# Kernel tuning notes

Measured on AMD Instinct MI355X. Metric: run time of the kernel, lower is better.

## Reference

```python
import jax, jax.numpy as jnp
import numpy as np

N, E = 20000, 320000
IN, HID, OUT, H = 128, 32, 1, 4
EPS = 1e-16  # PyG softmax epsilon


def _p(key, shape, scale=0.05):
    return jax.random.normal(key, shape, dtype=jnp.float32) * scale


def setup_inputs() -> dict:
    key = jax.random.key(0)
    ks = jax.random.split(key, 20)
    d = {
        "x": jax.random.normal(ks[0], (N, IN), dtype=jnp.float32),
        "edge_src": jax.random.randint(ks[1], (E,), 0, N, dtype=jnp.int32),
        "edge_dst": jax.random.randint(ks[2], (E,), 0, N, dtype=jnp.int32),
        # layer 1: TransformerConv(IN, HID, H)  ->  [N, H*HID]
        "W1q": _p(ks[3], (IN, H * HID)), "b1q": jnp.zeros((H * HID,), jnp.float32),
        "W1k": _p(ks[4], (IN, H * HID)), "b1k": jnp.zeros((H * HID,), jnp.float32),
        "W1v": _p(ks[5], (IN, H * HID)), "b1v": jnp.zeros((H * HID,), jnp.float32),
        "W1s": _p(ks[6], (IN, H * HID)), "b1s": jnp.zeros((H * HID,), jnp.float32),
        # layer 2: TransformerConv(H*HID, OUT, H) -> [N, H*OUT]
        "W2q": _p(ks[7], (H * HID, H * OUT)), "b2q": jnp.zeros((H * OUT,), jnp.float32),
        "W2k": _p(ks[8], (H * HID, H * OUT)), "b2k": jnp.zeros((H * OUT,), jnp.float32),
        "W2v": _p(ks[9], (H * HID, H * OUT)), "b2v": jnp.zeros((H * OUT,), jnp.float32),
        "W2s": _p(ks[10], (H * HID, H * OUT)), "b2s": jnp.zeros((H * OUT,), jnp.float32),
        # final nn.Linear(heads, 1)
        "Wl": _p(ks[11], (H, 1)), "bl": jnp.zeros((1,), jnp.float32),
    }
    return d


def transformer_conv(x, src, dst, Wq, bq, Wk, bk, Wv, bv, Ws, bs, heads, ch):
    n = x.shape[0]
    q = (x @ Wq + bq).reshape(n, heads, ch)
    k = (x @ Wk + bk).reshape(n, heads, ch)
    v = (x @ Wv + bv).reshape(n, heads, ch)
    qi, kj, vj = q[dst], k[src], v[src]            # [E,H,C] gathers
    score = (qi * kj).sum(-1) / jnp.sqrt(jnp.float32(ch))  # [E,H]
    m = jax.ops.segment_max(score, dst, num_segments=n)    # segment softmax by target
    e = jnp.exp(score - m[dst])
    s = jax.ops.segment_sum(e, dst, num_segments=n)
    alpha = e / (s[dst] + EPS)                              # [E,H]
    agg = jax.ops.segment_sum(alpha[:, :, None] * vj, dst, num_segments=n)  # [N,H,C]
    return agg.reshape(n, heads * ch) + x @ Ws + bs          # concat + root skip


def reference(x, edge_src, edge_dst,
              W1q, b1q, W1k, b1k, W1v, b1v, W1s, b1s,
              W2q, b2q, W2k, b2k, W2v, b2v, W2s, b2s,
              Wl, bl):
    h = transformer_conv(x, edge_src, edge_dst, W1q, b1q, W1k, b1k, W1v, b1v, W1s, b1s, H, HID)
    h = jax.nn.relu(h)  # dropout is identity in eval
    h = transformer_conv(h, edge_src, edge_dst, W2q, b2q, W2k, b2k, W2v, b2v, W2s, b2s, H, OUT)
    y = h @ Wl + bl                      # [N,1]
    return y.mean(axis=0, keepdims=True)  # [1,1]
```

## Files before the change

### kernel.cpp

```cpp
#include <hip/hip_runtime.h>
#include <math.h>

static constexpr float EPS_PYG = 1e-16f;
static constexpr float INV_SQRT32 = 0.17677669529663687f;

typedef short bf16x8 __attribute__((ext_vector_type(8)));
typedef float f32x4 __attribute__((ext_vector_type(4)));

__device__ inline unsigned short f2bf(float f) {
    union { float f; unsigned u; } x; x.f = f;
    unsigned r = x.u + 0x7FFFu + ((x.u >> 16) & 1u);
    return (unsigned short)(r >> 16);
}
__device__ inline float bf_hi(unsigned u) {
    union { unsigned u; float f; } x; x.u = u & 0xFFFF0000u; return x.f;
}
__device__ inline float bf_lo(unsigned u) {
    union { unsigned u; float f; } x; x.u = u << 16; return x.f;
}

__global__ void deg_slot_kernel(const int* __restrict__ dst, int* __restrict__ deg,
                                int* __restrict__ slot, int E) {
    int e = blockIdx.x * blockDim.x + threadIdx.x;
    if (e < E) slot[e] = atomicAdd(&deg[dst[e]], 1);
}

__global__ __launch_bounds__(1024) void scan_kernel(const int* __restrict__ deg,
                                                    int* __restrict__ row_off, int n,
                                                    float* __restrict__ out,
                                                    const float* __restrict__ bl) {
    const int t = threadIdx.x;
    const int CH = (n + 1023) >> 10;
    const int base = t * CH;
    int vals[32];
    int sum = 0;
#pragma unroll 4
    for (int i = 0; i < CH; ++i) {
        int idx = base + i;
        int v = (idx < n) ? deg[idx] : 0;
        sum += v;
        vals[i] = sum;
    }
    const int lane = t & 63;
    const int wid = t >> 6;
    int wsum = sum;
#pragma unroll
    for (int off = 1; off < 64; off <<= 1) {
        int o = __shfl_up(wsum, off, 64);
        if (lane >= off) wsum += o;
    }
    __shared__ int wtot[16];
    if (lane == 63) wtot[wid] = wsum;
    __syncthreads();
    if (t < 64) {
        int v = (t < 16) ? wtot[t] : 0;
        int inc = v;
#pragma unroll
        for (int off = 1; off < 16; off <<= 1) {
            int o = __shfl_up(inc, off, 64);
            if (t >= off) inc += o;
        }
        if (t < 16) wtot[t] = inc - v;
    }
    __syncthreads();
    const int toff = wtot[wid] + (wsum - sum);
    if (t == 0) { row_off[0] = 0; out[0] = bl[0]; }
#pragma unroll 4
    for (int i = 0; i < CH; ++i) {
        int idx = base + i;
        if (idx < n) row_off[idx + 1] = toff + vals[i];
    }
}

__global__ void scatter_kernel(const int* __restrict__ src, const int* __restrict__ dst,
                               const int* __restrict__ row_off, const int* __restrict__ slot,
                               int* __restrict__ csr_src, int E) {
    int e = blockIdx.x * blockDim.x + threadIdx.x;
    if (e < E) csr_src[row_off[dst[e]] + slot[e]] = src[e];
}

__global__ __launch_bounds__(256) void prep_kernel(
    const float4* __restrict__ X, ushort4* __restrict__ Xb, int total4,
    const float* __restrict__ Wq, const float* __restrict__ Wk,
    const float* __restrict__ Wv, const float* __restrict__ Wsk,
    unsigned short* __restrict__ Wbt)
{
    const int b = blockIdx.x;
    if (b < 4) {
        const float* W = (b == 0) ? Wq : (b == 1) ? Wk : (b == 2) ? Wv : Wsk;
        for (int i = threadIdx.x; i < 16384; i += 256) {
            int k = i >> 7, nn = i & 127;
            Wbt[b * 16384 + nn * 128 + k] = f2bf(W[i]);
        }
    } else {
        int i = (b - 4) * 256 + threadIdx.x;
        if (i < total4) {
            float4 v = X[i];
            ushort4 o;
            o.x = f2bf(v.x); o.y = f2bf(v.y); o.z = f2bf(v.z); o.w = f2bf(v.w);
            Xb[i] = o;
        }
    }
}

__global__ __launch_bounds__(256) void gemm1_mfma(
    const unsigned short* __restrict__ Xb, const unsigned short* __restrict__ Wbt,
    const float* __restrict__ bq, const float* __restrict__ bk,
    const float* __restrict__ bv, const float* __restrict__ bsk,
    float* __restrict__ Q, unsigned int* __restrict__ KV,
    float* __restrict__ S, int n)
{
    const int mode = blockIdx.y;

    const int tid  = threadIdx.x;
    const int wave = tid >> 6;
    const int lane = tid & 63;
    const int m    = lane & 15;
    const int quad = lane >> 4;
    const int r0   = blockIdx.x * 64 + wave * 16;

    int arow = r0 + m;
    if (arow >= n) arow = n - 1;

    if (mode == 1) {
        const unsigned short* WK = Wbt + 16384;
        const unsigned short* WV = Wbt + 2 * 16384;
        f32x4 accK[8] = {};
        f32x4 accV[8] = {};
#pragma unroll
        for (int kc = 0; kc < 128; kc += 32) {
            bf16x8 a = *(const bf16x8*)(Xb + (size_t)arow * 128 + kc + quad * 8);
#pragma unroll
            for (int ct = 0; ct < 8; ++ct) {
                bf16x8 bk8 = *(const bf16x8*)(WK + (ct * 16 + m) * 128 + kc + quad * 8);
                accK[ct] = __builtin_amdgcn_mfma_f32_16x16x32_bf16(a, bk8, accK[ct], 0, 0, 0);
                bf16x8 bv8 = *(const bf16x8*)(WV + (ct * 16 + m) * 128 + kc + quad * 8);
                accV[ct] = __builtin_amdgcn_mfma_f32_16x16x32_bf16(a, bv8, accV[ct], 0, 0, 0);
            }
        }
#pragma unroll
        for (int ct = 0; ct < 8; ++ct) {
            const int col = ct * 16 + m;
            const float bbk = bk[col], bbv = bv[col];
#pragma unroll
            for (int r = 0; r < 4; ++r) {
                const int row = r0 + quad * 4 + r;
                if (row < n) {
                    unsigned kb = f2bf(accK[ct][r] + bbk);
                    unsigned vb = f2bf(accV[ct][r] + bbv);
                    KV[(size_t)row * 128 + col] = (kb << 16) | vb;
                }
            }
        }
    } else {
        const int mat = (mode == 0) ? 0 : 3;
        const unsigned short* W = Wbt + (size_t)mat * 16384;
        const float* bias = (mode == 0) ? bq : bsk;
        float* C = (mode == 0) ? Q : S;
        f32x4 acc[8] = {};
#pragma unroll
        for (int kc = 0; kc < 128; kc += 32) {
            bf16x8 a = *(const bf16x8*)(Xb + (size_t)arow * 128 + kc + quad * 8);
#pragma unroll
            for (int ct = 0; ct < 8; ++ct) {
                bf16x8 bfr = *(const bf16x8*)(W + (ct * 16 + m) * 128 + kc + quad * 8);
                acc[ct] = __builtin_amdgcn_mfma_f32_16x16x32_bf16(a, bfr, acc[ct], 0, 0, 0);
            }
        }
#pragma unroll
        for (int ct = 0; ct < 8; ++ct) {
            const int col = ct * 16 + m;
            const float bb = bias[col];
#pragma unroll
            for (int r = 0; r < 4; ++r) {
                const int row = r0 + quad * 4 + r;
                if (row < n) C[(size_t)row * 128 + col] = acc[ct][r] + bb;
            }
        }
    }
}

__global__ __launch_bounds__(128) void l1_agg_kernel(
    const float* __restrict__ Q, const unsigned int* __restrict__ KV,
    const float* __restrict__ S,
    const int* __restrict__ row_off, const int* __restrict__ csr_src,
    float* __restrict__ H1, int n)
{
    const int node = blockIdx.x;
    const int t = threadIdx.x;
    const float q = Q[(size_t)node * 128 + t];
    const int beg = row_off[node], end = row_off[node + 1];

    float l = 0.f, acc = 0.f;
    int pos = beg;
    for (; pos + 4 <= end; pos += 4) {
        int s0 = csr_src[pos];
        int s1 = csr_src[pos + 1];
        int s2 = csr_src[pos + 2];
        int s3 = csr_src[pos + 3];
        unsigned u0 = KV[(size_t)s0 * 128 + t];
        unsigned u1 = KV[(size_t)s1 * 128 + t];
        unsigned u2 = KV[(size_t)s2 * 128 + t];
        unsigned u3 = KV[(size_t)s3 * 128 + t];
        float p0 = q * bf_hi(u0), p1 = q * bf_hi(u1);
        float p2 = q * bf_hi(u2), p3 = q * bf_hi(u3);
        p0 += __shfl_xor(p0, 16, 32); p1 += __shfl_xor(p1, 16, 32);
        p2 += __shfl_xor(p2, 16, 32); p3 += __shfl_xor(p3, 16, 32);
        p0 += __shfl_xor(p0, 8, 32);  p1 += __shfl_xor(p1, 8, 32);
        p2 += __shfl_xor(p2, 8, 32);  p3 += __shfl_xor(p3, 8, 32);
        p0 += __shfl_xor(p0, 4, 32);  p1 += __shfl_xor(p1, 4, 32);
        p2 += __shfl_xor(p2, 4, 32);  p3 += __shfl_xor(p3, 4, 32);
        p0 += __shfl_xor(p0, 2, 32);  p1 += __shfl_xor(p1, 2, 32);
        p2 += __shfl_xor(p2, 2, 32);  p3 += __shfl_xor(p3, 2, 32);
        p0 += __shfl_xor(p0, 1, 32);  p1 += __shfl_xor(p1, 1, 32);
        p2 += __shfl_xor(p2, 1, 32);  p3 += __shfl_xor(p3, 1, 32);
        float e0 = __expf(p0 * INV_SQRT32);
        float e1 = __expf(p1 * INV_SQRT32);
        float e2 = __expf(p2 * INV_SQRT32);
        float e3 = __expf(p3 * INV_SQRT32);
        l   += (e0 + e1) + (e2 + e3);
        acc += (e0 * bf_lo(u0) + e1 * bf_lo(u1)) + (e2 * bf_lo(u2) + e3 * bf_lo(u3));
    }
    for (; pos < end; ++pos) {
        int s0 = csr_src[pos];
        unsigned u0 = KV[(size_t)s0 * 128 + t];
        float p0 = q * bf_hi(u0);
        p0 += __shfl_xor(p0, 16, 32);
        p0 += __shfl_xor(p0, 8, 32);
        p0 += __shfl_xor(p0, 4, 32);
        p0 += __shfl_xor(p0, 2, 32);
        p0 += __shfl_xor(p0, 1, 32);
        float e0 = __expf(p0 * INV_SQRT32);
        l += e0;
        acc += e0 * bf_lo(u0);
    }
    float out = acc / (l + EPS_PYG) + S[(size_t)node * 128 + t];
    H1[(size_t)node * 128 + t] = fmaxf(out, 0.f);
}

__global__ __launch_bounds__(256) void gemm2_kernel(
    const float* __restrict__ H1,
    const float* __restrict__ Wq, const float* __restrict__ Wk,
    const float* __restrict__ Wv, const float* __restrict__ Wsk,
    const float* __restrict__ bq, const float* __restrict__ bk,
    const float* __restrict__ bv, const float* __restrict__ bsk,
    float4* __restrict__ Q2, float4* __restrict__ KV2, float4* __restrict__ S2, int n)
{
    __shared__ float Hs[64][129];
    __shared__ float Wt[128][16];
    __shared__ float bt[16];

    const int tid = threadIdx.x;
    const int r0 = blockIdx.x * 64;

    for (int i = tid; i < 2048; i += 256) {
        int row = i >> 4, col = i & 15;
        int mt = col >> 2, c = col & 3;
        const float* Wm = (mt == 0) ? Wq : (mt == 1) ? Wk : (mt == 2) ? Wv : Wsk;
        Wt[row][col] = Wm[row * 4 + c];
    }
    if (tid < 16) {
        int mt = tid >> 2;
        const float* bm = (mt == 0) ? bq : (mt == 1) ? bk : (mt == 2) ? bv : bsk;
        bt[tid] = bm[tid & 3];
    }
    for (int f = tid; f < 2048; f += 256) {
        int row = f >> 5, c4 = f & 31;
        float4 val = make_float4(0.f, 0.f, 0.f, 0.f);
        if (r0 + row < n) val = ((const float4*)H1)[(size_t)(r0 + row) * 32 + c4];
        Hs[row][c4 * 4 + 0] = val.x;
        Hs[row][c4 * 4 + 1] = val.y;
        Hs[row][c4 * 4 + 2] = val.z;
        Hs[row][c4 * 4 + 3] = val.w;
    }
    __syncthreads();

    const int nl = tid & 63;
    const int jg = tid >> 6;
    float a0 = 0.f, a1 = 0.f, a2 = 0.f, a3 = 0.f;
#pragma unroll 4
    for (int k = 0; k < 128; ++k) {
        float h = Hs[nl][k];
        a0 += h * Wt[k][jg * 4 + 0];
        a1 += h * Wt[k][jg * 4 + 1];
        a2 += h * Wt[k][jg * 4 + 2];
        a3 += h * Wt[k][jg * 4 + 3];
    }
    int node = r0 + nl;
    if (node < n) {
        float4 o = make_float4(a0 + bt[jg * 4 + 0], a1 + bt[jg * 4 + 1],
                               a2 + bt[jg * 4 + 2], a3 + bt[jg * 4 + 3]);
        if (jg == 0)      Q2[node] = o;
        else if (jg == 1) KV2[(size_t)node * 2 + 0] = o;
        else if (jg == 2) KV2[(size_t)node * 2 + 1] = o;
        else              S2[node] = o;
    }
}

__global__ __launch_bounds__(256) void l2_agg_kernel(
    const float4* __restrict__ Q2, const float4* __restrict__ KV2,
    const float4* __restrict__ S2,
    const int* __restrict__ row_off, const int* __restrict__ csr_src,
    const float* __restrict__ Wl, float* __restrict__ out, int n, float invn)
{
    const int t  = threadIdx.x;
    const int g  = t >> 4;
    const int gl = t & 15;
    const int nd = blockIdx.x * 16 + g;
    float y = 0.f;
    if (nd < n) {
        const int beg = row_off[nd], end = row_off[nd + 1];
        float4 q = Q2[nd];
        float l0 = 0.f, l1 = 0.f, l2 = 0.f, l3 = 0.f;
        float a0 = 0.f, a1 = 0.f, a2 = 0.f, a3 = 0.f;
        for (int pos = beg + gl; pos < end; pos += 16) {
            int src = csr_src[pos];
            float4 k = KV2[(size_t)src * 2 + 0];
            float4 v = KV2[(size_t)src * 2 + 1];
            float e0 = __expf(q.x * k.x);
            float e1 = __expf(q.y * k.y);
            float e2 = __expf(q.z * k.z);
            float e3 = __expf(q.w * k.w);
            l0 += e0; a0 += e0 * v.x;
            l1 += e1; a1 += e1 * v.y;
            l2 += e2; a2 += e2 * v.z;
            l3 += e3; a3 += e3 * v.w;
        }
#pragma unroll
        for (int mk = 8; mk >= 1; mk >>= 1) {
            l0 += __shfl_xor(l0, mk, 16); l1 += __shfl_xor(l1, mk, 16);
            l2 += __shfl_xor(l2, mk, 16); l3 += __shfl_xor(l3, mk, 16);
            a0 += __shfl_xor(a0, mk, 16); a1 += __shfl_xor(a1, mk, 16);
            a2 += __shfl_xor(a2, mk, 16); a3 += __shfl_xor(a3, mk, 16);
        }
        if (gl == 0) {
            float4 sk = S2[nd];
            float h0 = a0 / (l0 + EPS_PYG) + sk.x;
            float h1 = a1 / (l1 + EPS_PYG) + sk.y;
            float h2 = a2 / (l2 + EPS_PYG) + sk.z;
            float h3 = a3 / (l3 + EPS_PYG) + sk.w;
            y = (h0 * Wl[0] + h1 * Wl[1] + h2 * Wl[2] + h3 * Wl[3]) * invn;
        }
    }
    __shared__ float red[256];
    red[t] = y;
    __syncthreads();
    for (int off = 128; off > 0; off >>= 1) {
        if (t < (unsigned)off) red[t] += red[t + off];
        __syncthreads();
    }
    if (t == 0) atomicAdd(out, red[0]);
}

extern "C" void kernel_launch(void* const* d_in, const int* in_sizes, int n_in,
                              void* d_out, int out_size, void* d_ws, size_t ws_size,
                              hipStream_t stream) {
    const float* x        = (const float*)d_in[0];
    const int*   edge_src = (const int*)d_in[1];
    const int*   edge_dst = (const int*)d_in[2];
    const float* W1q = (const float*)d_in[3];  const float* b1q = (const float*)d_in[4];
    const float* W1k = (const float*)d_in[5];  const float* b1k = (const float*)d_in[6];
    const float* W1v = (const float*)d_in[7];  const float* b1v = (const float*)d_in[8];
    const float* W1s = (const float*)d_in[9];  const float* b1s = (const float*)d_in[10];
    const float* W2q = (const float*)d_in[11]; const float* b2q = (const float*)d_in[12];
    const float* W2k = (const float*)d_in[13]; const float* b2k = (const float*)d_in[14];
    const float* W2v = (const float*)d_in[15]; const float* b2v = (const float*)d_in[16];
    const float* W2s = (const float*)d_in[17]; const float* b2s = (const float*)d_in[18];
    const float* Wl  = (const float*)d_in[19]; const float* bl  = (const float*)d_in[20];

    const int N = in_sizes[0] / 128;
    const int E = in_sizes[1];
    float* out = (float*)d_out;

    float* ws  = (float*)d_ws;
    size_t off = 0;
    float*        Q1  = ws + off; off += (size_t)N * 128;
    unsigned int* KV  = (unsigned int*)(ws + off); off += (size_t)N * 128;
    float*        S1  = ws + off; off += (size_t)N * 128;
    float*        H1  = ws + off; off += (size_t)N * 128;
    float*        q2  = ws + off; off += (size_t)N * 4;
    float*        kv2 = ws + off; off += (size_t)N * 8;
    float*        s2  = ws + off; off += (size_t)N * 4;
    unsigned short* Xb  = (unsigned short*)(ws + off); off += (size_t)N * 64;
    unsigned short* Wbt = (unsigned short*)(ws + off); off += 4 * 16384 / 2;
    int* ibase   = (int*)(ws + off);
    int* deg     = ibase;
    int* row_off = ibase + N;
    int* slot    = ibase + 2 * N + 4;
    int* csr_src = slot + E;

    hipMemsetAsync(deg, 0, (size_t)N * sizeof(int), stream);
    deg_slot_kernel<<<(E + 255) / 256, 256, 0, stream>>>(edge_dst, deg, slot, E);
    scan_kernel<<<1, 1024, 0, stream>>>(deg, row_off, N, out, bl);
    scatter_kernel<<<(E + 255) / 256, 256, 0, stream>>>(edge_src, edge_dst, row_off,
                                                        slot, csr_src, E);

    const int total4 = N * 32;
    prep_kernel<<<4 + (total4 + 255) / 256, 256, 0, stream>>>(
        (const float4*)x, (ushort4*)Xb, total4, W1q, W1k, W1v, W1s, Wbt);

    {
        dim3 grid((N + 63) / 64, 3);
        gemm1_mfma<<<grid, 256, 0, stream>>>(Xb, Wbt, b1q, b1k, b1v, b1s,
                                             Q1, KV, S1, N);
    }
    l1_agg_kernel<<<N, 128, 0, stream>>>(Q1, KV, S1, row_off, csr_src, H1, N);

    gemm2_kernel<<<(N + 63) / 64, 256, 0, stream>>>(H1, W2q, W2k, W2v, W2s,
                                                    b2q, b2k, b2v, b2s,
                                                    (float4*)q2, (float4*)kv2,
                                                    (float4*)s2, N);
    l2_agg_kernel<<<(N + 15) / 16, 256, 0, stream>>>((const float4*)q2,
                                                     (const float4*)kv2,
                                                     (const float4*)s2,
                                                     row_off, csr_src, Wl, out, N,
                                                     1.0f / (float)N);
}
```

Baseline: 253.8 us.

## Merge graph-build and prep launches, vectorize layer-1 aggregation to 32 lanes per node

The degree/slot atomics are merged with the bf16 conversion of X and the weights into one launch. The CSR scatter is merged with the layer-1 MFMA GEMM into another, with the GEMM grid flattened onto blockIdx.x. This cuts four launches down to two and lets independent work overlap. The layer-1 aggregation now gives each node a 32-lane group, so 8 nodes share a block, and each lane loads 4 channels with uint4/float4 accesses. That shortens each per-edge dot-product reduction to 3 shuffles, at the cost of a smaller unroll and more registers per lane.

```diff
diff --git a/kernel.cpp b/kernel.cpp
--- a/kernel.cpp
+++ b/kernel.cpp
@@ -19,10 +19,35 @@
     union { unsigned u; float f; } x; x.u = u << 16; return x.f;
 }
 
-__global__ void deg_slot_kernel(const int* __restrict__ dst, int* __restrict__ deg,
-                                int* __restrict__ slot, int E) {
-    int e = blockIdx.x * blockDim.x + threadIdx.x;
-    if (e < E) slot[e] = atomicAdd(&deg[dst[e]], 1);
+__global__ __launch_bounds__(256) void build_prep_kernel(
+    const int* __restrict__ dst, int* __restrict__ deg, int* __restrict__ slot,
+    int E, int nblk_deg,
+    const float4* __restrict__ X, ushort4* __restrict__ Xb, int total4,
+    const float* __restrict__ Wq, const float* __restrict__ Wk,
+    const float* __restrict__ Wv, const float* __restrict__ Wsk,
+    unsigned short* __restrict__ Wbt)
+{
+    const int b = blockIdx.x;
+    const int t = threadIdx.x;
+    if (b < nblk_deg) {
+        int e = b * 256 + t;
+        if (e < E) slot[e] = atomicAdd(&deg[dst[e]], 1);
+    } else if (b < nblk_deg + 4) {
+        int m = b - nblk_deg;
+        const float* W = (m == 0) ? Wq : (m == 1) ? Wk : (m == 2) ? Wv : Wsk;
+        for (int i = t; i < 16384; i += 256) {
+            int k = i >> 7, nn = i & 127;
+            Wbt[m * 16384 + nn * 128 + k] = f2bf(W[i]);
+        }
+    } else {
+        int i = (b - nblk_deg - 4) * 256 + t;
+        if (i < total4) {
+            float4 v = X[i];
+            ushort4 o;
+            o.x = f2bf(v.x); o.y = f2bf(v.y); o.z = f2bf(v.z); o.w = f2bf(v.w);
+            Xb[i] = o;
+        }
+    }
 }
 
 __global__ __launch_bounds__(1024) void scan_kernel(const int* __restrict__ deg,
@@ -72,52 +97,32 @@
     }
 }
 
-__global__ void scatter_kernel(const int* __restrict__ src, const int* __restrict__ dst,
-                               const int* __restrict__ row_off, const int* __restrict__ slot,
-                               int* __restrict__ csr_src, int E) {
-    int e = blockIdx.x * blockDim.x + threadIdx.x;
-    if (e < E) csr_src[row_off[dst[e]] + slot[e]] = src[e];
-}
-
-__global__ __launch_bounds__(256) void prep_kernel(
-    const float4* __restrict__ X, ushort4* __restrict__ Xb, int total4,
-    const float* __restrict__ Wq, const float* __restrict__ Wk,
-    const float* __restrict__ Wv, const float* __restrict__ Wsk,
-    unsigned short* __restrict__ Wbt)
-{
-    const int b = blockIdx.x;
-    if (b < 4) {
-        const float* W = (b == 0) ? Wq : (b == 1) ? Wk : (b == 2) ? Wv : Wsk;
-        for (int i = threadIdx.x; i < 16384; i += 256) {
-            int k = i >> 7, nn = i & 127;
-            Wbt[b * 16384 + nn * 128 + k] = f2bf(W[i]);
-        }
-    } else {
-        int i = (b - 4) * 256 + threadIdx.x;
-        if (i < total4) {
-            float4 v = X[i];
-            ushort4 o;
-            o.x = f2bf(v.x); o.y = f2bf(v.y); o.z = f2bf(v.z); o.w = f2bf(v.w);
-            Xb[i] = o;
-        }
-    }
-}
-
-__global__ __launch_bounds__(256) void gemm1_mfma(
+__global__ __launch_bounds__(256) void scatter_gemm1_kernel(
+    const int* __restrict__ src, const int* __restrict__ dst,
+    const int* __restrict__ row_off, const int* __restrict__ slot,
+    int* __restrict__ csr_src, int E, int nblk_sc,
     const unsigned short* __restrict__ Xb, const unsigned short* __restrict__ Wbt,
     const float* __restrict__ bq, const float* __restrict__ bk,
     const float* __restrict__ bv, const float* __restrict__ bsk,
     float* __restrict__ Q, unsigned int* __restrict__ KV,
     float* __restrict__ S, int n)
 {
-    const int mode = blockIdx.y;
+    const int b = blockIdx.x;
+    if (b < nblk_sc) {
+        int e = b * 256 + threadIdx.x;
+        if (e < E) csr_src[row_off[dst[e]] + slot[e]] = src[e];
+        return;
+    }
+    const int g    = b - nblk_sc;
+    const int bx   = g / 3;
+    const int mode = g - bx * 3;
 
     const int tid  = threadIdx.x;
     const int wave = tid >> 6;
     const int lane = tid & 63;
     const int m    = lane & 15;
     const int quad = lane >> 4;
-    const int r0   = blockIdx.x * 64 + wave * 16;
+    const int r0   = bx * 64 + wave * 16;
 
     int arow = r0 + m;
     if (arow >= n) arow = n - 1;
@@ -180,62 +185,66 @@
     }
 }
 
-__global__ __launch_bounds__(128) void l1_agg_kernel(
+__global__ __launch_bounds__(256) void l1_agg_kernel(
     const float* __restrict__ Q, const unsigned int* __restrict__ KV,
     const float* __restrict__ S,
     const int* __restrict__ row_off, const int* __restrict__ csr_src,
     float* __restrict__ H1, int n)
 {
-    const int node = blockIdx.x;
     const int t = threadIdx.x;
-    const float q = Q[(size_t)node * 128 + t];
+    const int node = blockIdx.x * 8 + (t >> 5);
+    if (node >= n) return;
+    const int l = t & 31;
+    const int cbase = ((l >> 3) << 5) + ((l & 7) << 2);
+
+    const float4 q = *(const float4*)(Q + (size_t)node * 128 + cbase);
     const int beg = row_off[node], end = row_off[node + 1];
 
-    float l = 0.f, acc = 0.f;
+    float lsum = 0.f, a0 = 0.f, a1 = 0.f, a2 = 0.f, a3 = 0.f;
     int pos = beg;
-    for (; pos + 4 <= end; pos += 4) {
+    for (; pos + 2 <= end; pos += 2) {
         int s0 = csr_src[pos];
         int s1 = csr_src[pos + 1];
-        int s2 = csr_src[pos + 2];
-        int s3 = csr_src[pos + 3];
-        unsigned u0 = KV[(size_t)s0 * 128 + t];
-        unsigned u1 = KV[(size_t)s1 * 128 + t];
-        unsigned u2 = KV[(size_t)s2 * 128 + t];
-        unsigned u3 = KV[(size_t)s3 * 128 + t];
-        float p0 = q * bf_hi(u0), p1 = q * bf_hi(u1);
-        float p2 = q * bf_hi(u2), p3 = q * bf_hi(u3);
-        p0 += __shfl_xor(p0, 16, 32); p1 += __shfl_xor(p1, 16, 32);
-        p2 += __shfl_xor(p2, 16, 32); p3 += __shfl_xor(p3, 16, 32);
-        p0 += __shfl_xor(p0, 8, 32);  p1 += __shfl_xor(p1, 8, 32);
-        p2 += __shfl_xor(p2, 8, 32);  p3 += __shfl_xor(p3, 8, 32);
-        p0 += __shfl_xor(p0, 4, 32);  p1 += __shfl_xor(p1, 4, 32);
-        p2 += __shfl_xor(p2, 4, 32);  p3 += __shfl_xor(p3, 4, 32);
-        p0 += __shfl_xor(p0, 2, 32);  p1 += __shfl_xor(p1, 2, 32);
-        p2 += __shfl_xor(p2, 2, 32);  p3 += __shfl_xor(p3, 2, 32);
-        p0 += __shfl_xor(p0, 1, 32);  p1 += __shfl_xor(p1, 1, 32);
-        p2 += __shfl_xor(p2, 1, 32);  p3 += __shfl_xor(p3, 1, 32);
+        uint4 u0 = *(const uint4*)(KV + (size_t)s0 * 128 + cbase);
+        uint4 u1 = *(const uint4*)(KV + (size_t)s1 * 128 + cbase);
+        float p0 = q.x * bf_hi(u0.x) + q.y * bf_hi(u0.y)
+                 + q.z * bf_hi(u0.z) + q.w * bf_hi(u0.w);
+        float p1 = q.x * bf_hi(u1.x) + q.y * bf_hi(u1.y)
+                 + q.z * bf_hi(u1.z) + q.w * bf_hi(u1.w);
+        p0 += __shfl_xor(p0, 4, 8);  p1 += __shfl_xor(p1, 4, 8);
+        p0 += __shfl_xor(p0, 2, 8);  p1 += __shfl_xor(p1, 2, 8);
+        p0 += __shfl_xor(p0, 1, 8);  p1 += __shfl_xor(p1, 1, 8);
         float e0 = __expf(p0 * INV_SQRT32);
         float e1 = __expf(p1 * INV_SQRT32);
-        float e2 = __expf(p2 * INV_SQRT32);
-        float e3 = __expf(p3 * INV_SQRT32);
-        l   += (e0 + e1) + (e2 + e3);
-        acc += (e0 * bf_lo(u0) + e1 * bf_lo(u1)) + (e2 * bf_lo(u2) + e3 * bf_lo(u3));
-    }
-    for (; pos < end; ++pos) {
+        lsum += e0 + e1;
+        a0 += e0 * bf_lo(u0.x) + e1 * bf_lo(u1.x);
+        a1 += e0 * bf_lo(u0.y) + e1 * bf_lo(u1.y);
+        a2 += e0 * bf_lo(u0.z) + e1 * bf_lo(u1.z);
+        a3 += e0 * bf_lo(u0.w) + e1 * bf_lo(u1.w);
+    }
+    if (pos < end) {
         int s0 = csr_src[pos];
-        unsigned u0 = KV[(size_t)s0 * 128 + t];
-        float p0 = q * bf_hi(u0);
-        p0 += __shfl_xor(p0, 16, 32);
-        p0 += __shfl_xor(p0, 8, 32);
-        p0 += __shfl_xor(p0, 4, 32);
-        p0 += __shfl_xor(p0, 2, 32);
-        p0 += __shfl_xor(p0, 1, 32);
+        uint4 u0 = *(const uint4*)(KV + (size_t)s0 * 128 + cbase);
+        float p0 = q.x * bf_hi(u0.x) + q.y * bf_hi(u0.y)
+                 + q.z * bf_hi(u0.z) + q.w * bf_hi(u0.w);
+        p0 += __shfl_xor(p0, 4, 8);
+        p0 += __shfl_xor(p0, 2, 8);
+        p0 += __shfl_xor(p0, 1, 8);
         float e0 = __expf(p0 * INV_SQRT32);
-        l += e0;
-        acc += e0 * bf_lo(u0);
-    }
-    float out = acc / (l + EPS_PYG) + S[(size_t)node * 128 + t];
-    H1[(size_t)node * 128 + t] = fmaxf(out, 0.f);
+        lsum += e0;
+        a0 += e0 * bf_lo(u0.x);
+        a1 += e0 * bf_lo(u0.y);
+        a2 += e0 * bf_lo(u0.z);
+        a3 += e0 * bf_lo(u0.w);
+    }
+    const float inv = 1.0f / (lsum + EPS_PYG);
+    const float4 sk = *(const float4*)(S + (size_t)node * 128 + cbase);
+    float4 o;
+    o.x = fmaxf(a0 * inv + sk.x, 0.f);
+    o.y = fmaxf(a1 * inv + sk.y, 0.f);
+    o.z = fmaxf(a2 * inv + sk.z, 0.f);
+    o.w = fmaxf(a3 * inv + sk.w, 0.f);
+    *(float4*)(H1 + (size_t)node * 128 + cbase) = o;
 }
 
 __global__ __launch_bounds__(256) void gemm2_kernel(
@@ -389,27 +398,24 @@
     int* slot    = ibase + 2 * N + 4;
     int* csr_src = slot + E;
 
+    const int nblk_e = (E + 255) / 256;
+    const int total4 = N * 32;
+    const int nblk_x = (total4 + 255) / 256;
+    const int nblk_g = (N + 63) / 64;
+
     hipMemsetAsync(deg, 0, (size_t)N * sizeof(int), stream);
-    deg_slot_kernel<<<(E + 255) / 256, 256, 0, stream>>>(edge_dst, deg, slot, E);
+    build_prep_kernel<<<nblk_e + 4 + nblk_x, 256, 0, stream>>>(
+        edge_dst, deg, slot, E, nblk_e,
+        (const float4*)x, (ushort4*)Xb, total4, W1q, W1k, W1v, W1s, Wbt);
     scan_kernel<<<1, 1024, 0, stream>>>(deg, row_off, N, out, bl);
-    scatter_kernel<<<(E + 255) / 256, 256, 0, stream>>>(edge_src, edge_dst, row_off,
-                                                        slot, csr_src, E);
-
-    const int total4 = N * 32;
-    prep_kernel<<<4 + (total4 + 255) / 256, 256, 0, stream>>>(
-        (const float4*)x, (ushort4*)Xb, total4, W1q, W1k, W1v, W1s, Wbt);
-
-    {
-        dim3 grid((N + 63) / 64, 3);
-        gemm1_mfma<<<grid, 256, 0, stream>>>(Xb, Wbt, b1q, b1k, b1v, b1s,
-                                             Q1, KV, S1, N);
-    }
-    l1_agg_kernel<<<N, 128, 0, stream>>>(Q1, KV, S1, row_off, csr_src, H1, N);
-
-    gemm2_kernel<<<(N + 63) / 64, 256, 0, stream>>>(H1, W2q, W2k, W2v, W2s,
-                                                    b2q, b2k, b2v, b2s,
-                                                    (float4*)q2, (float4*)kv2,
-                                                    (float4*)s2, N);
+    scatter_gemm1_kernel<<<nblk_e + 3 * nblk_g, 256, 0, stream>>>(
+        edge_src, edge_dst, row_off, slot, csr_src, E, nblk_e,
+        Xb, Wbt, b1q, b1k, b1v, b1s, Q1, KV, S1, N);
+    l1_agg_kernel<<<(N + 7) / 8, 256, 0, stream>>>(Q1, KV, S1, row_off, csr_src, H1, N);
+    gemm2_kernel<<<nblk_g, 256, 0, stream>>>(H1, W2q, W2k, W2v, W2s,
+                                             b2q, b2k, b2v, b2s,
+                                             (float4*)q2, (float4*)kv2,
+                                             (float4*)s2, N);
     l2_agg_kernel<<<(N + 15) / 16, 256, 0, stream>>>((const float4*)q2,
                                                      (const float4*)kv2,
                                                      (const float4*)s2,
```

Measured after the change: 247.9 us. 1.02x faster.
